# Optimization experiments

Hardware: AMD Instinct MI355X
Metric: run time of the kernel (lower is better)

Reference implementation:

```python
import jax, jax.numpy as jnp
import numpy as np

N_ROUTES = 512
N_TIMES = 4096
N_MOVES = 16384
N_NODES = 2048
N_CDF = 8192
ALPHA, BETA = 0.15, 4


def setup_inputs() -> dict:
    key = jax.random.key(0)
    ks = jax.random.split(key, 7)
    x_raw = jax.random.normal(ks[0], (N_ROUTES, N_TIMES), dtype=jnp.float32)
    A = (jax.random.uniform(ks[1], (N_MOVES, N_ROUTES)) < 0.05).astype(jnp.float32)
    movement_node = jax.random.randint(ks[2], (N_MOVES,), 0, N_NODES, dtype=jnp.int32)
    cdf_node = jax.random.randint(ks[3], (N_CDF,), 0, N_NODES, dtype=jnp.int32)
    t_free = jax.random.uniform(ks[4], (N_CDF,), minval=0.5, maxval=2.0, dtype=jnp.float32)
    cap = jax.random.uniform(ks[5], (N_CDF,), minval=100.0, maxval=1000.0, dtype=jnp.float32)
    radio = jax.random.uniform(ks[6], (N_CDF,), minval=0.5, maxval=1.5, dtype=jnp.float32)
    return {
        "x_raw": x_raw, "A": A,
        "t_free": t_free, "cap": cap, "radio": radio,
        "movement_node": movement_node, "cdf_node": cdf_node,
        "n_nodes": N_NODES,
    }


def reference(x_raw, A, t_free, cap, radio, movement_node, cdf_node, n_nodes):
    # x = relu(param).clamp(min=0) -> relu is sufficient
    x = jax.nn.relu(x_raw)                                  # [R, T]
    c_pred = A @ x                                          # [M, T]
    # per-node flow: sum of all movement rows sharing the same node
    node_flow = jax.ops.segment_sum(c_pred, movement_node, num_segments=n_nodes)  # [N, T]
    flow = node_flow[cdf_node]                              # [C, T]
    # BPR congestion delay per c_df row
    ratio = jnp.clip(flow / cap[:, None], 1e-6)
    delay_cong = t_free[:, None] * ALPHA * radio[:, None] * ratio ** BETA
    y_rows = t_free[:, None] * radio[:, None] + delay_cong  # [C, T]
    y_l_t_hat = y_rows.sum(axis=0)                          # [T]
    return x, c_pred, y_l_t_hat
```

## Files before the change

### kernel.cpp

```cpp
#include <hip/hip_runtime.h>

#define N_ROUTES 512
#define N_TIMES  4096
#define N_MOVES  16384
#define N_NODES  2048
#define N_CDF    8192
#define ALPHA    0.15f
#define NODE_CAP 32

typedef unsigned short ushort_t;
typedef __attribute__((ext_vector_type(8))) short short8;
typedef __attribute__((ext_vector_type(4))) float floatx4;


__device__ inline ushort_t f2bf(float f) {
    union { float f; unsigned u; } v; v.f = f;
    unsigned r = (v.u + 0x7FFFu + ((v.u >> 16) & 1u)) >> 16;
    return (ushort_t)r;
}

__global__ __launch_bounds__(256) void relu_kernel(const float4* __restrict__ xr,
                                                   float4* __restrict__ xo, int n4) {
    int i = blockIdx.x * blockDim.x + threadIdx.x;
    if (i < n4) {
        float4 v = xr[i];
        v.x = fmaxf(v.x, 0.f); v.y = fmaxf(v.y, 0.f);
        v.z = fmaxf(v.z, 0.f); v.w = fmaxf(v.w, 0.f);
        xo[i] = v;
    }
}

__global__ __launch_bounds__(256) void transpose_bf(const float* __restrict__ xr,
                                                    ushort_t* __restrict__ xT) {
    __shared__ float ld[64][65];
    int t0 = blockIdx.x * 64;
    int k0 = blockIdx.y * 64;
    int tid = threadIdx.x;
    int col = tid & 63;
    #pragma unroll
    for (int i = 0; i < 16; ++i) {
        int row = i * 4 + (tid >> 6);
        ld[row][col] = fmaxf(xr[(size_t)(k0 + row) * N_TIMES + t0 + col], 0.f);
    }
    __syncthreads();
    int trow = tid >> 2;
    int kgrp = (tid & 3) * 16;
    ushort_t __align__(16) tmp[16];
    #pragma unroll
    for (int j = 0; j < 16; ++j) tmp[j] = f2bf(ld[kgrp + j][trow]);
    ushort_t* dst = xT + (size_t)(t0 + trow) * 512 + k0 + kgrp;
    *(uint4*)dst       = ((uint4*)tmp)[0];
    *(uint4*)(dst + 8) = ((uint4*)tmp)[1];
}

__global__ __launch_bounds__(256) void convA(const float* __restrict__ A,
                                             ushort_t* __restrict__ Ab) {
    size_t i = (size_t)(blockIdx.x * 256 + threadIdx.x) * 8;
    const float4* s = (const float4*)(A + i);
    float4 a = s[0], b = s[1];
    ushort_t __align__(16) t[8] = {f2bf(a.x), f2bf(a.y), f2bf(a.z), f2bf(a.w),
                                   f2bf(b.x), f2bf(b.y), f2bf(b.z), f2bf(b.w)};
    *(uint4*)(Ab + i) = *(uint4*)t;
}

__global__ __launch_bounds__(256) void build_nodes(const int* __restrict__ mnode,
                                                   int* __restrict__ ncnt,
                                                   int* __restrict__ nlist) {
    int m = blockIdx.x * blockDim.x + threadIdx.x;
    if (m >= N_MOVES) return;
    int n = mnode[m];
    int slot = atomicAdd(&ncnt[n], 1);
    if (slot < NODE_CAP) nlist[(size_t)n * NODE_CAP + slot] = m;
}

__global__ __launch_bounds__(128) void sa_kernel(const float* __restrict__ A,
                                                 const int* __restrict__ ncnt,
                                                 const int* __restrict__ nlist,
                                                 ushort_t* __restrict__ SAb) {
    int n = blockIdx.x, tid = threadIdx.x;
    int cnt = min(ncnt[n], NODE_CAP);
    float acc0 = 0.f, acc1 = 0.f, acc2 = 0.f, acc3 = 0.f;
    for (int j = 0; j < cnt; ++j) {
        int m = nlist[(size_t)n * NODE_CAP + j];
        float4 v = *(const float4*)(A + (size_t)m * 512 + tid * 4);
        acc0 += v.x; acc1 += v.y; acc2 += v.z; acc3 += v.w;
    }
    ushort_t __align__(8) t[4] = {f2bf(acc0), f2bf(acc1), f2bf(acc2), f2bf(acc3)};
    *(uint2*)(SAb + (size_t)n * 512 + tid * 4) = *(uint2*)t;
}

__global__ __launch_bounds__(256) void wsum_kernel(const float* __restrict__ t_free,
                                                   const float* __restrict__ cap,
                                                   const float* __restrict__ radio,
                                                   const int* __restrict__ cdf_node,
                                                   float* __restrict__ w,
                                                   float* __restrict__ basep) {
    int c = blockIdx.x * 256 + threadIdx.x;
    float tr = t_free[c] * radio[c];
    float ic = 1.0f / cap[c];
    float ic2 = ic * ic;
    atomicAdd(&w[cdf_node[c]], ALPHA * tr * ic2 * ic2);
    float b = tr;
    #pragma unroll
    for (int d = 32; d >= 1; d >>= 1) b += __shfl_down(b, d);
    if ((threadIdx.x & 63) == 0) atomicAdd(basep, b);
}

__global__ __launch_bounds__(256) void y_init(const float* __restrict__ basep,
                                              float* __restrict__ y) {
    y[blockIdx.x * 256 + threadIdx.x] = *basep;
}

#define GLOAD_LDS16(g, l) __builtin_amdgcn_global_load_lds( \
    (const __attribute__((address_space(1))) void*)(g),     \
    (__attribute__((address_space(3))) void*)(l), 16, 0, 0)

__global__ __launch_bounds__(256) void gemm_fused(const ushort_t* __restrict__ Abig,
                                                  const ushort_t* __restrict__ Bbf,
                                                  float* __restrict__ c_pred,
                                                  const float* __restrict__ w,
                                                  float* __restrict__ y) {
    __shared__ __align__(16) ushort_t Atile[128 * 64];
    __shared__ __align__(16) ushort_t Btile[128 * 64];

    const int tid  = threadIdx.x;
    const int wv   = tid >> 6;
    const int lane = tid & 63;
    const int quad = lane >> 4;
    const int l16  = lane & 15;
    const int bn   = blockIdx.x;
    const int bm   = blockIdx.y;

    const int mi = (wv & 1) * 64;
    const int ni = (wv >> 1) * 64;

    floatx4 acc[4][4] = {};

    const int srow  = lane >> 3;
    const int schk  = lane & 7;

    for (int kt = 0; kt < 8; ++kt) {
        if (kt) __syncthreads();
        #pragma unroll
        for (int c = 0; c < 4; ++c) {
            int rowbase = wv * 32 + c * 8;
            int row = rowbase + srow;
            int cl  = schk ^ (row & 7);
            const ushort_t* ga = Abig + (size_t)(bm * 128 + row) * 512 + kt * 64 + cl * 8;
            GLOAD_LDS16(ga, Atile + rowbase * 64);
            const ushort_t* gb = Bbf + (size_t)(bn * 128 + row) * 512 + kt * 64 + cl * 8;
            GLOAD_LDS16(gb, Btile + rowbase * 64);
        }
        __syncthreads();

        #pragma unroll
        for (int kk = 0; kk < 2; ++kk) {
            short8 af[4], bf[4];
            #pragma unroll
            for (int fi = 0; fi < 4; ++fi) {
                int row = mi + fi * 16 + l16;
                int cp  = (kk * 4 + quad) ^ (row & 7);
                af[fi] = *(const short8*)(Atile + row * 64 + cp * 8);
            }
            #pragma unroll
            for (int fj = 0; fj < 4; ++fj) {
                int row = ni + fj * 16 + l16;
                int cp  = (kk * 4 + quad) ^ (row & 7);
                bf[fj] = *(const short8*)(Btile + row * 64 + cp * 8);
            }
            #pragma unroll
            for (int fi = 0; fi < 4; ++fi)
                #pragma unroll
                for (int fj = 0; fj < 4; ++fj)
                    acc[fi][fj] = __builtin_amdgcn_mfma_f32_16x16x32_bf16(
                        af[fi], bf[fj], acc[fi][fj], 0, 0, 0);
        }
    }

    if (bm < 128) {
        #pragma unroll
        for (int fi = 0; fi < 4; ++fi) {
            #pragma unroll
            for (int reg = 0; reg < 4; ++reg) {
                size_t row = (size_t)bm * 128 + mi + fi * 16 + quad * 4 + reg;
                float* cp = c_pred + row * N_TIMES + bn * 128 + ni + l16;
                #pragma unroll
                for (int fj = 0; fj < 4; ++fj)
                    cp[fj * 16] = acc[fi][fj][reg];
            }
        }
    } else {
        int nb = (bm - 128) * 128;
        float psum[4] = {0.f, 0.f, 0.f, 0.f};
        #pragma unroll
        for (int fj = 0; fj < 4; ++fj)
            #pragma unroll
            for (int fi = 0; fi < 4; ++fi)
                #pragma unroll
                for (int reg = 0; reg < 4; ++reg) {
                    int n = nb + mi + fi * 16 + quad * 4 + reg;
                    float f = acc[fi][fj][reg];
                    float f2 = f * f;
                    psum[fj] += w[n] * f2 * f2;
                }
        #pragma unroll
        for (int fj = 0; fj < 4; ++fj) {
            float v = psum[fj];
            v += __shfl_xor(v, 16);
            v += __shfl_xor(v, 32);
            if (quad == 0)
                atomicAdd(&y[bn * 128 + ni + fj * 16 + l16], v);
        }
    }
}

extern "C" void kernel_launch(void* const* d_in, const int* in_sizes, int n_in,
                              void* d_out, int out_size, void* d_ws, size_t ws_size,
                              hipStream_t stream) {
    const float* x_raw         = (const float*)d_in[0];
    const float* A             = (const float*)d_in[1];
    const float* t_free        = (const float*)d_in[2];
    const float* cap           = (const float*)d_in[3];
    const float* radio         = (const float*)d_in[4];
    const int*   movement_node = (const int*)d_in[5];
    const int*   cdf_node      = (const int*)d_in[6];

    float* out    = (float*)d_out;
    float* x_out  = out;
    float* c_pred = out + (size_t)N_ROUTES * N_TIMES;
    float* y      = c_pred + (size_t)N_MOVES * N_TIMES;

    char* ws = (char*)d_ws;
    ushort_t* Abig  = (ushort_t*)(ws);
    ushort_t* SAb   = Abig + (size_t)N_MOVES * 512;
    ushort_t* xTbf  = (ushort_t*)(ws + 18874368);
    int*      ncnt  = (int*)(ws + 23068672);
    int*      nlist = (int*)(ws + 23076864);
    float*    w     = (float*)(ws + 23339008);
    float*    basep = (float*)(ws + 23347200);

    hipMemsetAsync(ncnt, 0, N_NODES * sizeof(int), stream);
    hipMemsetAsync(w, 0, N_NODES * sizeof(float), stream);
    hipMemsetAsync(basep, 0, sizeof(float), stream);

    relu_kernel<<<dim3((N_ROUTES * N_TIMES / 4 + 255) / 256), dim3(256), 0, stream>>>(
        (const float4*)x_raw, (float4*)x_out, N_ROUTES * N_TIMES / 4);

    transpose_bf<<<dim3(N_TIMES / 64, N_ROUTES / 64), dim3(256), 0, stream>>>(x_raw, xTbf);

    convA<<<dim3((int)((size_t)N_MOVES * 512 / 8 / 256)), dim3(256), 0, stream>>>(A, Abig);

    build_nodes<<<dim3(N_MOVES / 256), dim3(256), 0, stream>>>(movement_node, ncnt, nlist);

    sa_kernel<<<dim3(N_NODES), dim3(128), 0, stream>>>(A, ncnt, nlist, SAb);

    wsum_kernel<<<dim3(N_CDF / 256), dim3(256), 0, stream>>>(
        t_free, cap, radio, cdf_node, w, basep);

    y_init<<<dim3(N_TIMES / 256), dim3(256), 0, stream>>>(basep, y);

    gemm_fused<<<dim3(N_TIMES / 128, (N_MOVES + N_NODES) / 128), dim3(256), 0, stream>>>(
        Abig, xTbf, c_pred, w, y);
}
```

Before: 404.7 us.

## Double-buffer GEMM LDS tiles and fuse relu output into transpose kernel

The GEMM main loop now uses two LDS buffers per operand and issues the global-to-LDS loads for the next K tile before computing on the current one. This leaves one barrier per iteration and lets load latency overlap with MFMA work. LDS use doubles to 64KB per block, which may lower occupancy. Separately, the standalone relu kernel is removed and the transpose kernel writes the relu output directly, saving one launch and one extra read of x_raw.

```diff
diff --git a/kernel.cpp b/kernel.cpp
--- a/kernel.cpp
+++ b/kernel.cpp
@@ -19,18 +19,8 @@
     return (ushort_t)r;
 }
 
-__global__ __launch_bounds__(256) void relu_kernel(const float4* __restrict__ xr,
-                                                   float4* __restrict__ xo, int n4) {
-    int i = blockIdx.x * blockDim.x + threadIdx.x;
-    if (i < n4) {
-        float4 v = xr[i];
-        v.x = fmaxf(v.x, 0.f); v.y = fmaxf(v.y, 0.f);
-        v.z = fmaxf(v.z, 0.f); v.w = fmaxf(v.w, 0.f);
-        xo[i] = v;
-    }
-}
-
 __global__ __launch_bounds__(256) void transpose_bf(const float* __restrict__ xr,
+                                                    float* __restrict__ xo,
                                                     ushort_t* __restrict__ xT) {
     __shared__ float ld[64][65];
     int t0 = blockIdx.x * 64;
@@ -40,7 +30,9 @@
     #pragma unroll
     for (int i = 0; i < 16; ++i) {
         int row = i * 4 + (tid >> 6);
-        ld[row][col] = fmaxf(xr[(size_t)(k0 + row) * N_TIMES + t0 + col], 0.f);
+        float v = fmaxf(xr[(size_t)(k0 + row) * N_TIMES + t0 + col], 0.f);
+        ld[row][col] = v;
+        xo[(size_t)(k0 + row) * N_TIMES + t0 + col] = v;
     }
     __syncthreads();
     int trow = tid >> 2;
@@ -120,8 +112,8 @@
                                                   float* __restrict__ c_pred,
                                                   const float* __restrict__ w,
                                                   float* __restrict__ y) {
-    __shared__ __align__(16) ushort_t Atile[128 * 64];
-    __shared__ __align__(16) ushort_t Btile[128 * 64];
+    __shared__ __align__(16) ushort_t Atile[2][128 * 64];
+    __shared__ __align__(16) ushort_t Btile[2][128 * 64];
 
     const int tid  = threadIdx.x;
     const int wv   = tid >> 6;
@@ -136,22 +128,33 @@
 
     floatx4 acc[4][4] = {};
 
-    const int srow  = lane >> 3;
-    const int schk  = lane & 7;
-
+    const int srow = lane >> 3;
+    const int schk = lane & 7;
+
+    const ushort_t* gA = Abig + (size_t)(bm * 128) * 512;
+    const ushort_t* gB = Bbf  + (size_t)(bn * 128) * 512;
+
+#define STAGE(buf, kt)                                                       \
+    {                                                                        \
+        _Pragma("unroll")                                                    \
+        for (int c = 0; c < 4; ++c) {                                        \
+            int rowbase = wv * 32 + c * 8;                                   \
+            int row = rowbase + srow;                                        \
+            int cl  = schk ^ (row & 7);                                      \
+            GLOAD_LDS16(gA + (size_t)row * 512 + (kt) * 64 + cl * 8,         \
+                        &Atile[buf][rowbase * 64]);                          \
+            GLOAD_LDS16(gB + (size_t)row * 512 + (kt) * 64 + cl * 8,         \
+                        &Btile[buf][rowbase * 64]);                          \
+        }                                                                    \
+    }
+
+    STAGE(0, 0);
+    __syncthreads();
+
+    int cur = 0;
+    #pragma unroll
     for (int kt = 0; kt < 8; ++kt) {
-        if (kt) __syncthreads();
-        #pragma unroll
-        for (int c = 0; c < 4; ++c) {
-            int rowbase = wv * 32 + c * 8;
-            int row = rowbase + srow;
-            int cl  = schk ^ (row & 7);
-            const ushort_t* ga = Abig + (size_t)(bm * 128 + row) * 512 + kt * 64 + cl * 8;
-            GLOAD_LDS16(ga, Atile + rowbase * 64);
-            const ushort_t* gb = Bbf + (size_t)(bn * 128 + row) * 512 + kt * 64 + cl * 8;
-            GLOAD_LDS16(gb, Btile + rowbase * 64);
-        }
-        __syncthreads();
+        if (kt < 7) STAGE(cur ^ 1, kt + 1);
 
         #pragma unroll
         for (int kk = 0; kk < 2; ++kk) {
@@ -160,13 +163,13 @@
             for (int fi = 0; fi < 4; ++fi) {
                 int row = mi + fi * 16 + l16;
                 int cp  = (kk * 4 + quad) ^ (row & 7);
-                af[fi] = *(const short8*)(Atile + row * 64 + cp * 8);
+                af[fi] = *(const short8*)(&Atile[cur][row * 64 + cp * 8]);
             }
             #pragma unroll
             for (int fj = 0; fj < 4; ++fj) {
                 int row = ni + fj * 16 + l16;
                 int cp  = (kk * 4 + quad) ^ (row & 7);
-                bf[fj] = *(const short8*)(Btile + row * 64 + cp * 8);
+                bf[fj] = *(const short8*)(&Btile[cur][row * 64 + cp * 8]);
             }
             #pragma unroll
             for (int fi = 0; fi < 4; ++fi)
@@ -175,7 +178,13 @@
                     acc[fi][fj] = __builtin_amdgcn_mfma_f32_16x16x32_bf16(
                         af[fi], bf[fj], acc[fi][fj], 0, 0, 0);
         }
-    }
+
+        if (kt < 7) {
+            __syncthreads();
+            cur ^= 1;
+        }
+    }
+#undef STAGE
 
     if (bm < 128) {
         #pragma unroll
@@ -243,10 +252,8 @@
     hipMemsetAsync(w, 0, N_NODES * sizeof(float), stream);
     hipMemsetAsync(basep, 0, sizeof(float), stream);
 
-    relu_kernel<<<dim3((N_ROUTES * N_TIMES / 4 + 255) / 256), dim3(256), 0, stream>>>(
-        (const float4*)x_raw, (float4*)x_out, N_ROUTES * N_TIMES / 4);
-
-    transpose_bf<<<dim3(N_TIMES / 64, N_ROUTES / 64), dim3(256), 0, stream>>>(x_raw, xTbf);
+    transpose_bf<<<dim3(N_TIMES / 64, N_ROUTES / 64), dim3(256), 0, stream>>>(
+        x_raw, x_out, xTbf);
 
     convA<<<dim3((int)((size_t)N_MOVES * 512 / 8 / 256)), dim3(256), 0, stream>>>(A, Abig);
 
```

Result: slower. 412.9 us (+2.0%).
